# Kernel tuning notes

Measured on AMD Instinct MI355X. Metric: run time of the kernel, lower is better.

The kernel has to match this reference:

```python
import jax, jax.numpy as jnp
import numpy as np

V, E, D, B, T = 50000, 128, 512, 256, 128


def _reverse_seq(x, lengths):
    # TF reverse_sequence: reverse only the valid prefix of each row.
    Tn = x.shape[1]
    t = jnp.arange(Tn)
    idx = jnp.where(t[None, :] < lengths[:, None], lengths[:, None] - 1 - t[None, :], t[None, :])
    return jnp.take_along_axis(x, idx[:, :, None], axis=1)


def _lstm(x, lengths, Wx, Wh, b, reverse):
    # x: [B,T,in]; returns outputs [B,T,D] (zero past length) and final cell state [B,D]
    if reverse:
        x = _reverse_seq(x, lengths)
    Bn, Tn, _ = x.shape
    Dn = Wh.shape[0]
    xg = jnp.einsum('btd,dg->tbg', x, Wx) + b  # [T,B,4D], input projection hoisted out of scan

    def step(carry, inp):
        h, c = carry
        xg_t, t = inp
        gates = xg_t + h @ Wh
        i, j, f, o = jnp.split(gates, 4, axis=-1)  # TF LSTMCell gate order i, j, f, o
        c_new = jax.nn.sigmoid(f + 1.0) * c + jax.nn.sigmoid(i) * jnp.tanh(j)  # forget_bias=1.0
        h_new = jax.nn.sigmoid(o) * jnp.tanh(c_new)
        mask = (t < lengths)[:, None]
        c2 = jnp.where(mask, c_new, c)
        h2 = jnp.where(mask, h_new, h)
        out = jnp.where(mask, h_new, 0.0)  # dynamic_rnn zeros outputs past length
        return (h2, c2), out

    init = (jnp.zeros((Bn, Dn), x.dtype), jnp.zeros((Bn, Dn), x.dtype))
    (h, c), outs = jax.lax.scan(step, init, (xg, jnp.arange(Tn)))
    outs = outs.transpose(1, 0, 2)  # [B,T,D]
    if reverse:
        outs = _reverse_seq(outs, lengths)
    return outs, c


def setup_inputs() -> dict:
    key = jax.random.key(0)
    ks = jax.random.split(key, 20)
    s = 0.05
    inp = {
        'tokens': jax.random.randint(ks[0], (B, T), 0, V, dtype=jnp.int32),
        'lengths': jax.random.randint(ks[1], (B,), 1, T + 1, dtype=jnp.int32),
        'embedding': jax.random.normal(ks[2], (V, E), jnp.float32) * s,
    }
    in_dims = [E, 2 * D]
    k = 3
    for l in range(2):
        for d in ('f', 'b'):
            inp[f'Wx_{d}{l}'] = jax.random.normal(ks[k], (in_dims[l], 4 * D), jnp.float32) * s; k += 1
            inp[f'Wh_{d}{l}'] = jax.random.normal(ks[k], (D, 4 * D), jnp.float32) * s; k += 1
            inp[f'b_{d}{l}'] = jnp.zeros((4 * D,), jnp.float32)
    inp['W_head'] = jax.random.normal(ks[k], (2 * D, D), jnp.float32) * s; k += 1
    inp['b1'] = jnp.zeros((D,), jnp.float32)
    inp['U'] = jax.random.normal(ks[k], (D, V), jnp.float32) * s; k += 1
    inp['b2'] = jnp.zeros((V,), jnp.float32)
    return inp


def reference(tokens, lengths, embedding, Wx_f0, Wh_f0, b_f0, Wx_b0, Wh_b0, b_b0,
              Wx_f1, Wh_f1, b_f1, Wx_b1, Wh_b1, b_b1, W_head, b1, U, b2):
    x = embedding[tokens]  # [B,T,E]
    fw_out, fw_c = _lstm(x, lengths, Wx_f0, Wh_f0, b_f0, reverse=False)
    bw_out, bw_c = _lstm(x, lengths, Wx_b0, Wh_b0, b_b0, reverse=True)
    x = jnp.concatenate([fw_out, bw_out], axis=-1)  # [B,T,2D]
    fw_out, fw_c = _lstm(x, lengths, Wx_f1, Wh_f1, b_f1, reverse=False)
    bw_out, bw_c = _lstm(x, lengths, Wx_b1, Wh_b1, b_b1, reverse=True)
    states = jnp.concatenate([fw_c, bw_c], axis=-1)  # top-layer final cell states [B,2D]
    h = jax.nn.relu(states @ W_head + b1)
    pred = h @ U + b2  # [B,V]
    return pred
```

## Files before the change

kernel.cpp:

```cpp
#include <hip/hip_runtime.h>
#include <hip/hip_bf16.h>
#include <stdint.h>


#define DEV static __device__ __forceinline__

using f32x4 = __attribute__((ext_vector_type(4))) float;
using s16x8 = __attribute__((ext_vector_type(8))) short;
typedef unsigned long long u64;

#define TT 128
#define DD 512
#define VV 50000

#define O_CTR0   ((size_t)0)
#define O_CTR1   ((size_t)2048)
#define O_HG0    ((size_t)4096)
#define SZ_HG    ((size_t)(2*8*64*512*2))
#define O_HG1    (O_HG0 + SZ_HG)
#define O_ZEND   (O_HG1 + SZ_HG)
#define O_XEMB   (O_ZEND)
#define O_W0T    (O_XEMB + (size_t)32768*128*2)
#define O_WH1T   (O_W0T  + (size_t)2*2048*640*2)
#define O_W1XT   (O_WH1T + (size_t)2*2048*512*2)
#define O_WHDT   (O_W1XT + (size_t)4096*1024*2)
#define O_STATES (O_WHDT + (size_t)512*1024*2)
#define O_HHEAD  (O_STATES + (size_t)256*1024*2)
#define O_OUT0   (O_HHEAD + (size_t)256*512*2)
#define O_XG1    (O_OUT0 + (size_t)32768*1024*2)
#define THIN_END (O_XG1 + (size_t)32768*2048*2)
#define FAT_END  (O_XG1 + (size_t)32768*4096*2)

DEV unsigned short f2bf(float f) {
  union { float f; unsigned int u; } a; a.f = f;
  unsigned int r = a.u + 0x7FFFu + ((a.u >> 16) & 1u);
  return (unsigned short)(r >> 16);
}
DEV float bf2f(unsigned short u) {
  union { unsigned int u; float f; } a; a.u = ((unsigned int)u) << 16; return a.f;
}
DEV float sigm(float x)  { return __builtin_amdgcn_rcpf(1.f + __expf(-x)); }
DEV float tanh_(float x) { return 1.f - 2.f * __builtin_amdgcn_rcpf(1.f + __expf(2.f * x)); }

DEV void gload16(const void* g, void* l) {
  __builtin_amdgcn_global_load_lds((const __attribute__((address_space(1))) void*)g,
                                   (__attribute__((address_space(3))) void*)l, 16, 0, 0);
}

__global__ __launch_bounds__(256) void k_embed(const int* __restrict__ tok,
                                               const float* __restrict__ emb,
                                               unsigned short* __restrict__ x) {
  for (int i = blockIdx.x * 256 + threadIdx.x; i < 32768 * 16; i += 256 * 256) {
    int bt = i >> 4, c = i & 15;
    int tk = tok[bt];
    const float* s = emb + (size_t)tk * 128 + c * 8;
    float4 a = *(const float4*)s, b = *(const float4*)(s + 4);
    union { unsigned short us[8]; s16x8 v; } o;
    o.us[0] = f2bf(a.x); o.us[1] = f2bf(a.y); o.us[2] = f2bf(a.z); o.us[3] = f2bf(a.w);
    o.us[4] = f2bf(b.x); o.us[5] = f2bf(b.y); o.us[6] = f2bf(b.z); o.us[7] = f2bf(b.w);
    *(s16x8*)&x[(size_t)bt * 128 + c * 8] = o.v;
  }
}

__global__ __launch_bounds__(256) void k_prep(const float* __restrict__ src,
                                              unsigned short* __restrict__ dst,
                                              int k_off, int src_ld, int K_full,
                                              int perm, int swz) {
  __shared__ __align__(16) unsigned short tile[64][72];
  int n0 = blockIdx.x * 64, k0 = blockIdx.y * 64;
  int t = threadIdx.x;
  for (int r = 0; r < 16; ++r) {
    int kk = r * 4 + (t >> 6);
    int nn = t & 63;
    int n = n0 + nn;
    int col = perm ? (((n >> 4) & 3) * 512 + (n >> 6) * 16 + (n & 15)) : n;
    tile[nn][kk] = f2bf(src[(size_t)(k0 + kk) * src_ld + col]);
  }
  __syncthreads();
  for (int j = 0; j < 2; ++j) {
    int ch = j * 256 + t;
    int nn = ch >> 3, kc = ch & 7;
    s16x8 v = *(const s16x8*)&tile[nn][kc * 8];
    int n = n0 + nn;
    size_t byte = ((size_t)n * K_full + (k_off + k0 + kc * 8)) * 2;
    if (swz) byte ^= (size_t)((n & 7) << 4);
    *(s16x8*)((char*)dst + byte) = v;
  }
}

DEV void poll_ctr(const int* p, int target) {
  if ((threadIdx.x & 63) == 0) {
    int guard = 0;
    while (__hip_atomic_load(p, __ATOMIC_RELAXED, __HIP_MEMORY_SCOPE_AGENT) < target) {
      __builtin_amdgcn_s_sleep(1);
      if (++guard > (1 << 18)) break;
    }
  }
  asm volatile("" ::: "memory");
}
DEV void arrive_ctr(int* p) {
  __syncthreads();
  if (threadIdx.x == 0)
    __hip_atomic_fetch_add(p, 1, __ATOMIC_RELAXED, __HIP_MEMORY_SCOPE_AGENT);
}

DEV u64 hload8(const void* p) {
  return __hip_atomic_load((const u64*)p, __ATOMIC_RELAXED, __HIP_MEMORY_SCOPE_AGENT);
}
DEV void hstore_pair(unsigned short* addr_even, float hv, int lane) {
  unsigned int hb = (unsigned int)f2bf(hv);
  unsigned int pb = __shfl_xor(hb, 1);
  if (!(lane & 1))
    __hip_atomic_store((unsigned int*)addr_even, hb | (pb << 16),
                       __ATOMIC_RELAXED, __HIP_MEMORY_SCOPE_AGENT);
}

__global__ __launch_bounds__(256) void k_lstm0(
    const unsigned short* __restrict__ xemb, const unsigned short* __restrict__ W0T,
    const int* __restrict__ lengths, const float* __restrict__ bf0,
    const float* __restrict__ bb0, unsigned short* __restrict__ hg,
    int* __restrict__ ctr, unsigned short* __restrict__ out0) {
  extern __shared__ char smem[];
  int bid = blockIdx.x;
  int combo = bid & 7, chunk = bid >> 3;
  int dir = combo >> 2, grp = combo & 3;
  int tid = threadIdx.x;
  {
    const char* wsrc = (const char*)W0T + ((size_t)(dir * 2048 + chunk * 64)) * 640 * 2;
    for (int j = 0; j < 20; ++j)
      gload16(wsrc + j * 4096 + tid * 16, smem + j * 4096 + (tid >> 6) * 1024);
  }
  __syncthreads();

  int lane = tid & 63, l15 = lane & 15, lhi = lane >> 4, m = tid >> 6;
  int rowAl = m * 16 + l15;
  int rowA = grp * 64 + rowAl;
  int lenA = lengths[rowA];
  int dim = chunk * 16 + l15;
  const float* bs = dir ? bb0 : bf0;
  float bias[4];
  #pragma unroll
  for (int g = 0; g < 4; ++g) bias[g] = bs[g * 512 + dim];

  int rpl[4], lenP[4];
  #pragma unroll
  for (int r = 0; r < 4; ++r) {
    rpl[r] = m * 16 + lhi * 4 + r;
    lenP[r] = lengths[grp * 64 + rpl[r]];
  }
  float cS[4] = {0.f, 0.f, 0.f, 0.f};
  float hP[4] = {0.f, 0.f, 0.f, 0.f};
  int X = (l15 & 7) << 4;
  int bn[4];
  #pragma unroll
  for (int g = 0; g < 4; ++g) bn[g] = (g * 16 + l15) * 1280 + lhi * 16;
  int* ctr_p = ctr + combo * 16;

  for (int t = 0; t < TT; ++t) {
    int posA = dir ? ((t < lenA) ? lenA - 1 - t : t) : t;
    const char* xb = (const char*)xemb + ((size_t)(rowA * 128 + posA)) * 128 * 2;
    s16x8 xf[4];
    #pragma unroll
    for (int kt = 0; kt < 4; ++kt)
      xf[kt] = *(const s16x8*)(xb + (kt * 32 + lhi * 8) * 2);

    poll_ctr(ctr_p, 32 * t);
    const char* hr = (const char*)hg + ((size_t)((t & 1) * 8 + combo)) * 64 * 512 * 2
                     + (size_t)rowAl * 512 * 2;
    u64 h8[32];
    #pragma unroll
    for (int kt = 0; kt < 16; ++kt) {
      h8[2 * kt]     = hload8(hr + kt * 64 + lhi * 16);
      h8[2 * kt + 1] = hload8(hr + kt * 64 + lhi * 16 + 8);
    }
    f32x4 acc[4] = {};
    #pragma unroll
    for (int kt = 0; kt < 20; ++kt) {
      s16x8 a;
      if (kt < 4) a = xf[kt];
      else { union { u64 q[2]; s16x8 v; } u;
             u.q[0] = h8[2 * (kt - 4)]; u.q[1] = h8[2 * (kt - 4) + 1]; a = u.v; }
      #pragma unroll
      for (int g = 0; g < 4; ++g) {
        s16x8 b = *(const s16x8*)(smem + ((bn[g] + kt * 64) ^ X));
        acc[g] = __builtin_amdgcn_mfma_f32_16x16x32_bf16(a, b, acc[g], 0, 0, 0);
      }
    }
    unsigned short* hw = hg + ((size_t)(((t + 1) & 1) * 8 + combo)) * 64 * 512;
    #pragma unroll
    for (int r = 0; r < 4; ++r) {
      float gi = acc[0][r] + bias[0];
      float gj = acc[1][r] + bias[1];
      float gf = acc[2][r] + bias[2];
      float go = acc[3][r] + bias[3];
      float cn = sigm(gf + 1.f) * cS[r] + sigm(gi) * tanh_(gj);
      float hn = sigm(go) * tanh_(cn);
      int act = (t < lenP[r]);
      cS[r] = act ? cn : cS[r];
      float hv = act ? hn : hP[r];
      hP[r] = hv;
      hstore_pair(&hw[rpl[r] * 512 + (dim & ~1)], hv, lane);
      int b = grp * 64 + rpl[r];
      int posP = dir ? ((act) ? lenP[r] - 1 - t : t) : t;
      out0[((size_t)b * 128 + posP) * 1024 + dir * 512 + dim] = f2bf(act ? hn : 0.f);
    }
    arrive_ctr(ctr_p);
  }
}

__global__ __launch_bounds__(256) void k_lstm1(
    const unsigned short* __restrict__ xg, int ldxg, int dircolmul,
    const unsigned short* __restrict__ Wh1T, const int* __restrict__ lengths,
    const float* __restrict__ bf1, const float* __restrict__ bb1,
    unsigned short* __restrict__ hg, int* __restrict__ ctr,
    unsigned short* __restrict__ states, int dirFixed) {
  extern __shared__ char smem[];
  int bid = blockIdx.x;
  int dir, grp, chunk;
  if (dirFixed >= 0) { dir = dirFixed; grp = bid & 3; chunk = bid >> 2; }
  else               { dir = (bid & 7) >> 2; grp = bid & 3; chunk = bid >> 3; }
  int combo = dir * 4 + grp;
  int tid = threadIdx.x;
  {
    const char* wsrc = (const char*)Wh1T + ((size_t)(dir * 2048 + chunk * 64)) * 512 * 2;
    for (int j = 0; j < 16; ++j)
      gload16(wsrc + j * 4096 + tid * 16, smem + j * 4096 + (tid >> 6) * 1024);
  }
  __syncthreads();

  int lane = tid & 63, l15 = lane & 15, lhi = lane >> 4, m = tid >> 6;
  int rowAl = m * 16 + l15;
  int dim = chunk * 16 + l15;
  const float* bs = dir ? bb1 : bf1;
  float bias[4];
  #pragma unroll
  for (int g = 0; g < 4; ++g) bias[g] = bs[g * 512 + dim];
  int rpl[4], lenP[4], bG[4];
  #pragma unroll
  for (int r = 0; r < 4; ++r) {
    rpl[r] = m * 16 + lhi * 4 + r;
    bG[r] = grp * 64 + rpl[r];
    lenP[r] = lengths[bG[r]];
  }
  float cS[4] = {0.f, 0.f, 0.f, 0.f};
  float hP[4] = {0.f, 0.f, 0.f, 0.f};
  int X = (l15 & 7) << 4;
  int bn[4];
  #pragma unroll
  for (int g = 0; g < 4; ++g) bn[g] = (g * 16 + l15) * 1024 + lhi * 16;
  int* ctr_p = ctr + combo * 16;
  int colbase = dircolmul * dir + chunk * 64 + l15;

  for (int t = 0; t < TT; ++t) {
    unsigned short xv[4][4];
    #pragma unroll
    for (int r = 0; r < 4; ++r) {
      int posP = dir ? ((t < lenP[r]) ? lenP[r] - 1 - t : t) : t;
      size_t rowoff = ((size_t)bG[r] * 128 + posP) * ldxg + colbase;
      #pragma unroll
      for (int g = 0; g < 4; ++g) xv[g][r] = xg[rowoff + g * 16];
    }
    poll_ctr(ctr_p, 32 * t);
    const char* hr = (const char*)hg + ((size_t)((t & 1) * 8 + combo)) * 64 * 512 * 2
                     + (size_t)rowAl * 512 * 2;
    u64 h8[32];
    #pragma unroll
    for (int kt = 0; kt < 16; ++kt) {
      h8[2 * kt]     = hload8(hr + kt * 64 + lhi * 16);
      h8[2 * kt + 1] = hload8(hr + kt * 64 + lhi * 16 + 8);
    }
    f32x4 acc[4] = {};
    #pragma unroll
    for (int kt = 0; kt < 16; ++kt) {
      union { u64 q[2]; s16x8 v; } u;
      u.q[0] = h8[2 * kt]; u.q[1] = h8[2 * kt + 1];
      s16x8 a = u.v;
      #pragma unroll
      for (int g = 0; g < 4; ++g) {
        s16x8 b = *(const s16x8*)(smem + ((bn[g] + kt * 64) ^ X));
        acc[g] = __builtin_amdgcn_mfma_f32_16x16x32_bf16(a, b, acc[g], 0, 0, 0);
      }
    }
    unsigned short* hw = hg + ((size_t)(((t + 1) & 1) * 8 + combo)) * 64 * 512;
    #pragma unroll
    for (int r = 0; r < 4; ++r) {
      float gi = acc[0][r] + bias[0] + bf2f(xv[0][r]);
      float gj = acc[1][r] + bias[1] + bf2f(xv[1][r]);
      float gf = acc[2][r] + bias[2] + bf2f(xv[2][r]);
      float go = acc[3][r] + bias[3] + bf2f(xv[3][r]);
      float cn = sigm(gf + 1.f) * cS[r] + sigm(gi) * tanh_(gj);
      float hn = sigm(go) * tanh_(cn);
      int act = (t < lenP[r]);
      cS[r] = act ? cn : cS[r];
      float hv = act ? hn : hP[r];
      hP[r] = hv;
      hstore_pair(&hw[rpl[r] * 512 + (dim & ~1)], hv, lane);
    }
    arrive_ctr(ctr_p);
  }
  #pragma unroll
  for (int r = 0; r < 4; ++r)
    states[(size_t)bG[r] * 1024 + dir * 512 + dim] = f2bf(cS[r]);
}

__global__ __launch_bounds__(256) void k_gemm(const unsigned short* __restrict__ A,
                                              const unsigned short* __restrict__ Bt,
                                              unsigned short* __restrict__ C,
                                              int K, int ldc, int mode,
                                              const float* __restrict__ bias) {
  __shared__ __align__(16) char gs[65536];
  int m0 = blockIdx.x * 128, n0 = blockIdx.y * 128;
  int tid = threadIdx.x, lane = tid & 63, l15 = lane & 15, lhi = lane >> 4;
  int w = tid >> 6, wrow = w >> 1, wcol = w & 1;
  f32x4 acc[4][4] = {};
  int nk = K >> 6;

  auto stage = [&](int buf, int ki) {
    const char* As = (const char*)A + ((size_t)m0 * K + ki * 64) * 2;
    const char* Bs = (const char*)Bt + ((size_t)n0 * K + ki * 64) * 2;
    for (int j = 0; j < 4; ++j) {
      int fb = j * 4096 + tid * 16;
      int row = fb >> 7, inrow = fb & 127;
      gload16(As + (size_t)row * K * 2 + inrow, gs + buf * 16384 + j * 4096 + (tid >> 6) * 1024);
      gload16(Bs + (size_t)row * K * 2 + inrow, gs + 32768 + buf * 16384 + j * 4096 + (tid >> 6) * 1024);
    }
  };
  stage(0, 0);
  __syncthreads();
  for (int ki = 0; ki < nk; ++ki) {
    int buf = ki & 1;
    if (ki + 1 < nk) stage(buf ^ 1, ki + 1);
    const char* sa = gs + buf * 16384;
    const char* sb = gs + 32768 + buf * 16384;
    #pragma unroll
    for (int kt = 0; kt < 2; ++kt) {
      s16x8 af[4];
      #pragma unroll
      for (int mt = 0; mt < 4; ++mt)
        af[mt] = *(const s16x8*)(sa + ((wrow * 64 + mt * 16 + l15) * 128 + kt * 64 + lhi * 16));
      #pragma unroll
      for (int nt = 0; nt < 4; ++nt) {
        s16x8 bf_ = *(const s16x8*)(sb + ((wcol * 64 + nt * 16 + l15) * 128 + kt * 64 + lhi * 16));
        #pragma unroll
        for (int mt = 0; mt < 4; ++mt)
          acc[mt][nt] = __builtin_amdgcn_mfma_f32_16x16x32_bf16(af[mt], bf_, acc[mt][nt], 0, 0, 0);
      }
    }
    __syncthreads();
  }
  #pragma unroll
  for (int mt = 0; mt < 4; ++mt)
    #pragma unroll
    for (int nt = 0; nt < 4; ++nt)
      #pragma unroll
      for (int r = 0; r < 4; ++r) {
        int row = m0 + wrow * 64 + mt * 16 + lhi * 4 + r;
        int col = n0 + wcol * 64 + nt * 16 + l15;
        float v = acc[mt][nt][r];
        if (mode) { v += bias[col]; v = fmaxf(v, 0.f); }
        C[(size_t)row * ldc + col] = f2bf(v);
      }
}

__global__ __launch_bounds__(256) void k_pred(const unsigned short* __restrict__ hh,
                                              const float* __restrict__ U,
                                              const float* __restrict__ b2,
                                              float* __restrict__ out) {
  __shared__ __align__(16) char ps[65536];
  int n0 = blockIdx.x * 128;
  int tid = threadIdx.x, lane = tid & 63, l15 = lane & 15, lhi = lane >> 4, w = tid >> 6;
  f32x4 acc[4][8] = {};
  unsigned short* tb = (unsigned short*)(ps + 32768);
  bool full = (n0 + 128) <= VV;

  for (int ki = 0; ki < 8; ++ki) {
    int k0 = ki * 64;
    const char* As = (const char*)hh + (size_t)k0 * 2;
    for (int j = 0; j < 8; ++j) {
      int fb = j * 4096 + tid * 16;
      int row = fb >> 7, inrow = fb & 127;
      gload16(As + (size_t)row * 512 * 2 + inrow, ps + j * 4096 + (tid >> 6) * 1024);
    }
    for (int c8 = 0; c8 < 8; ++c8) {
      int flat = c8 * 1024 + tid * 4;
      int kk = flat >> 7, nn = flat & 127;
      float v0, v1, v2, v3;
      if (full) {
        float4 v = *(const float4*)(U + (size_t)(k0 + kk) * VV + (n0 + nn));
        v0 = v.x; v1 = v.y; v2 = v.z; v3 = v.w;
      } else {
        v0 = (n0 + nn + 0 < VV) ? U[(size_t)(k0 + kk) * VV + n0 + nn + 0] : 0.f;
        v1 = (n0 + nn + 1 < VV) ? U[(size_t)(k0 + kk) * VV + n0 + nn + 1] : 0.f;
        v2 = (n0 + nn + 2 < VV) ? U[(size_t)(k0 + kk) * VV + n0 + nn + 2] : 0.f;
        v3 = (n0 + nn + 3 < VV) ? U[(size_t)(k0 + kk) * VV + n0 + nn + 3] : 0.f;
      }
      tb[(nn + 0) * 72 + kk] = f2bf(v0);
      tb[(nn + 1) * 72 + kk] = f2bf(v1);
      tb[(nn + 2) * 72 + kk] = f2bf(v2);
      tb[(nn + 3) * 72 + kk] = f2bf(v3);
    }
    __syncthreads();
    #pragma unroll
    for (int kt = 0; kt < 2; ++kt) {
      s16x8 af[4];
      #pragma unroll
      for (int mt = 0; mt < 4; ++mt)
        af[mt] = *(const s16x8*)(ps + ((w * 64 + mt * 16 + l15) * 128 + kt * 64 + lhi * 16));
      #pragma unroll
      for (int nt = 0; nt < 8; ++nt) {
        s16x8 bf_ = *(const s16x8*)((char*)tb + ((nt * 16 + l15) * 144 + kt * 64 + lhi * 16));
        #pragma unroll
        for (int mt = 0; mt < 4; ++mt)
          acc[mt][nt] = __builtin_amdgcn_mfma_f32_16x16x32_bf16(af[mt], bf_, acc[mt][nt], 0, 0, 0);
      }
    }
    __syncthreads();
  }
  #pragma unroll
  for (int nt = 0; nt < 8; ++nt) {
    int col = n0 + nt * 16 + l15;
    float bv = (col < VV) ? b2[col] : 0.f;
    #pragma unroll
    for (int mt = 0; mt < 4; ++mt)
      #pragma unroll
      for (int r = 0; r < 4; ++r) {
        int row = w * 64 + mt * 16 + lhi * 4 + r;
        if (col < VV) out[(size_t)row * VV + col] = acc[mt][nt][r] + bv;
      }
  }
}

extern "C" void kernel_launch(void* const* d_in, const int* in_sizes, int n_in,
                              void* d_out, int out_size, void* d_ws, size_t ws_size,
                              hipStream_t stream) {
  const int* tokens = (const int*)d_in[0];
  const int* lengths = (const int*)d_in[1];
  const float* emb   = (const float*)d_in[2];
  const float* Wx_f0 = (const float*)d_in[3];
  const float* Wh_f0 = (const float*)d_in[4];
  const float* b_f0  = (const float*)d_in[5];
  const float* Wx_b0 = (const float*)d_in[6];
  const float* Wh_b0 = (const float*)d_in[7];
  const float* b_b0  = (const float*)d_in[8];
  const float* Wx_f1 = (const float*)d_in[9];
  const float* Wh_f1 = (const float*)d_in[10];
  const float* b_f1  = (const float*)d_in[11];
  const float* Wx_b1 = (const float*)d_in[12];
  const float* Wh_b1 = (const float*)d_in[13];
  const float* b_b1  = (const float*)d_in[14];
  const float* W_head = (const float*)d_in[15];
  const float* b1    = (const float*)d_in[16];
  const float* U     = (const float*)d_in[17];
  const float* b2    = (const float*)d_in[18];

  if (ws_size < (size_t)THIN_END) return;

  char* ws = (char*)d_ws;
  int* ctr0 = (int*)(ws + O_CTR0);
  int* ctr1 = (int*)(ws + O_CTR1);
  unsigned short* hg0   = (unsigned short*)(ws + O_HG0);
  unsigned short* hg1   = (unsigned short*)(ws + O_HG1);
  unsigned short* xemb  = (unsigned short*)(ws + O_XEMB);
  unsigned short* W0T   = (unsigned short*)(ws + O_W0T);
  unsigned short* WH1T  = (unsigned short*)(ws + O_WH1T);
  unsigned short* W1XT  = (unsigned short*)(ws + O_W1XT);
  unsigned short* WHDT  = (unsigned short*)(ws + O_WHDT);
  unsigned short* states = (unsigned short*)(ws + O_STATES);
  unsigned short* hhead = (unsigned short*)(ws + O_HHEAD);
  unsigned short* out0  = (unsigned short*)(ws + O_OUT0);
  unsigned short* xg1   = (unsigned short*)(ws + O_XG1);

  bool fat = (ws_size >= (size_t)FAT_END);

  hipFuncSetAttribute((const void*)k_lstm0, hipFuncAttributeMaxDynamicSharedMemorySize, 81920);
  hipFuncSetAttribute((const void*)k_lstm1, hipFuncAttributeMaxDynamicSharedMemorySize, 65536);

  hipMemsetAsync(ws, 0, O_ZEND, stream);

  k_embed<<<dim3(256), dim3(256), 0, stream>>>(tokens, emb, xemb);

  k_prep<<<dim3(32, 2), 256, 0, stream>>>(Wx_f0, W0T,               0,   2048, 640, 1, 1);
  k_prep<<<dim3(32, 8), 256, 0, stream>>>(Wh_f0, W0T,               128, 2048, 640, 1, 1);
  k_prep<<<dim3(32, 2), 256, 0, stream>>>(Wx_b0, W0T + 2048 * 640,  0,   2048, 640, 1, 1);
  k_prep<<<dim3(32, 8), 256, 0, stream>>>(Wh_b0, W0T + 2048 * 640,  128, 2048, 640, 1, 1);
  k_prep<<<dim3(32, 8), 256, 0, stream>>>(Wh_f1, WH1T,              0,   2048, 512, 1, 1);
  k_prep<<<dim3(32, 8), 256, 0, stream>>>(Wh_b1, WH1T + 2048 * 512, 0,   2048, 512, 1, 1);
  k_prep<<<dim3(32, 16), 256, 0, stream>>>(Wx_f1, W1XT,               0, 2048, 1024, 1, 0);
  k_prep<<<dim3(32, 16), 256, 0, stream>>>(Wx_b1, W1XT + 2048 * 1024, 0, 2048, 1024, 1, 0);
  k_prep<<<dim3(8, 16), 256, 0, stream>>>(W_head, WHDT,              0,  512, 1024, 0, 0);

  k_lstm0<<<256, 256, 81920, stream>>>(xemb, W0T, lengths, b_f0, b_b0, hg0, ctr0, out0);

  if (fat) {
    k_gemm<<<dim3(256, 32), 256, 0, stream>>>(out0, W1XT, xg1, 1024, 4096, 0, nullptr);
    k_lstm1<<<256, 256, 65536, stream>>>(xg1, 4096, 2048, WH1T, lengths, b_f1, b_b1,
                                         hg1, ctr1, states, -1);
  } else {
    k_gemm<<<dim3(256, 16), 256, 0, stream>>>(out0, W1XT, xg1, 1024, 2048, 0, nullptr);
    k_lstm1<<<128, 256, 65536, stream>>>(xg1, 2048, 0, WH1T, lengths, b_f1, b_b1,
                                         hg1, ctr1, states, 0);
    k_gemm<<<dim3(256, 16), 256, 0, stream>>>(out0, W1XT + (size_t)2048 * 1024, xg1,
                                              1024, 2048, 0, nullptr);
    k_lstm1<<<128, 256, 65536, stream>>>(xg1, 2048, 0, WH1T, lengths, b_f1, b_b1,
                                         hg1, ctr1, states, 1);
  }

  k_gemm<<<dim3(2, 4), 256, 0, stream>>>(states, WHDT, hhead, 1024, 512, 1, b1);
  k_pred<<<dim3(391), 256, 0, stream>>>(hhead, U, b2, (float*)d_out);
}
```

Baseline: 2.260 ms.

## Replace counter barrier with per-wave flag sync and pack layer-1 gate loads

The shared atomic counter with block-wide syncthreads is replaced by per-wave, per-chunk flags that are stored after a vmcnt wait and polled with a wave-wide all-reduce. Each wave now waits only on the matching wave rows from other chunks, not on a whole-block barrier. The out0 store in layer 0 is moved after the flag publish, taking it off the critical path. The layer-1 input-projection weights are permuted so each lane's four gate values sit next to each other and can be fetched with one 64-bit load instead of 16 scalar loads. The risks are heavier polling traffic from 32 lanes spinning without sleep, and the correctness of the relaxed-ordering memory visibility.

```diff
diff --git a/kernel.cpp b/kernel.cpp
--- a/kernel.cpp
+++ b/kernel.cpp
@@ -14,8 +14,8 @@
 #define VV 50000
 
 #define O_CTR0   ((size_t)0)
-#define O_CTR1   ((size_t)2048)
-#define O_HG0    ((size_t)4096)
+#define O_CTR1   ((size_t)4096)
+#define O_HG0    ((size_t)8192)
 #define SZ_HG    ((size_t)(2*8*64*512*2))
 #define O_HG1    (O_HG0 + SZ_HG)
 #define O_ZEND   (O_HG1 + SZ_HG)
@@ -73,7 +73,9 @@
     int kk = r * 4 + (t >> 6);
     int nn = t & 63;
     int n = n0 + nn;
-    int col = perm ? (((n >> 4) & 3) * 512 + (n >> 6) * 16 + (n & 15)) : n;
+    int col = n;
+    if (perm == 1) col = ((n >> 4) & 3) * 512 + (n >> 6) * 16 + (n & 15);
+    if (perm == 2) col = (n & 3) * 512 + (n >> 6) * 16 + ((n >> 2) & 15);
     tile[nn][kk] = f2bf(src[(size_t)(k0 + kk) * src_ld + col]);
   }
   __syncthreads();
@@ -88,20 +90,20 @@
   }
 }
 
-DEV void poll_ctr(const int* p, int target) {
-  if ((threadIdx.x & 63) == 0) {
-    int guard = 0;
-    while (__hip_atomic_load(p, __ATOMIC_RELAXED, __HIP_MEMORY_SCOPE_AGENT) < target) {
-      __builtin_amdgcn_s_sleep(1);
-      if (++guard > (1 << 18)) break;
-    }
+DEV void poll_flags(const int* fbase, int target) {
+  const int* p = fbase + (threadIdx.x & 31);
+  int guard = 0;
+  for (;;) {
+    int v = __hip_atomic_load(p, __ATOMIC_RELAXED, __HIP_MEMORY_SCOPE_AGENT);
+    if (__all(v >= target)) break;
+    if (++guard > (1 << 18)) break;
   }
   asm volatile("" ::: "memory");
 }
-DEV void arrive_ctr(int* p) {
-  __syncthreads();
-  if (threadIdx.x == 0)
-    __hip_atomic_fetch_add(p, 1, __ATOMIC_RELAXED, __HIP_MEMORY_SCOPE_AGENT);
+DEV void set_flag(int* fp, int v, int lane) {
+  asm volatile("s_waitcnt vmcnt(0)" ::: "memory");
+  if (lane == 0)
+    __hip_atomic_store(fp, v, __ATOMIC_RELAXED, __HIP_MEMORY_SCOPE_AGENT);
 }
 
 DEV u64 hload8(const void* p) {
@@ -119,7 +121,7 @@
     const unsigned short* __restrict__ xemb, const unsigned short* __restrict__ W0T,
     const int* __restrict__ lengths, const float* __restrict__ bf0,
     const float* __restrict__ bb0, unsigned short* __restrict__ hg,
-    int* __restrict__ ctr, unsigned short* __restrict__ out0) {
+    int* __restrict__ flags, unsigned short* __restrict__ out0) {
   extern __shared__ char smem[];
   int bid = blockIdx.x;
   int combo = bid & 7, chunk = bid >> 3;
@@ -154,7 +156,8 @@
   int bn[4];
   #pragma unroll
   for (int g = 0; g < 4; ++g) bn[g] = (g * 16 + l15) * 1280 + lhi * 16;
-  int* ctr_p = ctr + combo * 16;
+  int* fbase = flags + (combo * 4 + m) * 32;
+  int* fown  = fbase + chunk;
 
   for (int t = 0; t < TT; ++t) {
     int posA = dir ? ((t < lenA) ? lenA - 1 - t : t) : t;
@@ -164,7 +167,7 @@
     for (int kt = 0; kt < 4; ++kt)
       xf[kt] = *(const s16x8*)(xb + (kt * 32 + lhi * 8) * 2);
 
-    poll_ctr(ctr_p, 32 * t);
+    poll_flags(fbase, t);
     const char* hr = (const char*)hg + ((size_t)((t & 1) * 8 + combo)) * 64 * 512 * 2
                      + (size_t)rowAl * 512 * 2;
     u64 h8[32];
@@ -187,6 +190,7 @@
       }
     }
     unsigned short* hw = hg + ((size_t)(((t + 1) & 1) * 8 + combo)) * 64 * 512;
+    float hnv[4]; int actv[4];
     #pragma unroll
     for (int r = 0; r < 4; ++r) {
       float gi = acc[0][r] + bias[0];
@@ -196,15 +200,19 @@
       float cn = sigm(gf + 1.f) * cS[r] + sigm(gi) * tanh_(gj);
       float hn = sigm(go) * tanh_(cn);
       int act = (t < lenP[r]);
+      hnv[r] = hn; actv[r] = act;
       cS[r] = act ? cn : cS[r];
       float hv = act ? hn : hP[r];
       hP[r] = hv;
       hstore_pair(&hw[rpl[r] * 512 + (dim & ~1)], hv, lane);
+    }
+    set_flag(fown, t + 1, lane);
+    #pragma unroll
+    for (int r = 0; r < 4; ++r) {
       int b = grp * 64 + rpl[r];
-      int posP = dir ? ((act) ? lenP[r] - 1 - t : t) : t;
-      out0[((size_t)b * 128 + posP) * 1024 + dir * 512 + dim] = f2bf(act ? hn : 0.f);
-    }
-    arrive_ctr(ctr_p);
+      int posP = dir ? (actv[r] ? lenP[r] - 1 - t : t) : t;
+      out0[((size_t)b * 128 + posP) * 1024 + dir * 512 + dim] = f2bf(actv[r] ? hnv[r] : 0.f);
+    }
   }
 }
 
@@ -212,7 +220,7 @@
     const unsigned short* __restrict__ xg, int ldxg, int dircolmul,
     const unsigned short* __restrict__ Wh1T, const int* __restrict__ lengths,
     const float* __restrict__ bf1, const float* __restrict__ bb1,
-    unsigned short* __restrict__ hg, int* __restrict__ ctr,
+    unsigned short* __restrict__ hg, int* __restrict__ flags,
     unsigned short* __restrict__ states, int dirFixed) {
   extern __shared__ char smem[];
   int bid = blockIdx.x;
@@ -248,19 +256,18 @@
   int bn[4];
   #pragma unroll
   for (int g = 0; g < 4; ++g) bn[g] = (g * 16 + l15) * 1024 + lhi * 16;
-  int* ctr_p = ctr + combo * 16;
-  int colbase = dircolmul * dir + chunk * 64 + l15;
+  int* fbase = flags + (combo * 4 + m) * 32;
+  int* fown  = fbase + chunk;
+  int colbase = dircolmul * dir + chunk * 64 + l15 * 4;
 
   for (int t = 0; t < TT; ++t) {
-    unsigned short xv[4][4];
+    u64 xq[4];
     #pragma unroll
     for (int r = 0; r < 4; ++r) {
       int posP = dir ? ((t < lenP[r]) ? lenP[r] - 1 - t : t) : t;
-      size_t rowoff = ((size_t)bG[r] * 128 + posP) * ldxg + colbase;
-      #pragma unroll
-      for (int g = 0; g < 4; ++g) xv[g][r] = xg[rowoff + g * 16];
-    }
-    poll_ctr(ctr_p, 32 * t);
+      xq[r] = *(const u64*)&xg[((size_t)bG[r] * 128 + posP) * ldxg + colbase];
+    }
+    poll_flags(fbase, t);
     const char* hr = (const char*)hg + ((size_t)((t & 1) * 8 + combo)) * 64 * 512 * 2
                      + (size_t)rowAl * 512 * 2;
     u64 h8[32];
@@ -284,10 +291,10 @@
     unsigned short* hw = hg + ((size_t)(((t + 1) & 1) * 8 + combo)) * 64 * 512;
     #pragma unroll
     for (int r = 0; r < 4; ++r) {
-      float gi = acc[0][r] + bias[0] + bf2f(xv[0][r]);
-      float gj = acc[1][r] + bias[1] + bf2f(xv[1][r]);
-      float gf = acc[2][r] + bias[2] + bf2f(xv[2][r]);
-      float go = acc[3][r] + bias[3] + bf2f(xv[3][r]);
+      float gi = acc[0][r] + bias[0] + bf2f((unsigned short)(xq[r]       & 0xFFFF));
+      float gj = acc[1][r] + bias[1] + bf2f((unsigned short)((xq[r]>>16) & 0xFFFF));
+      float gf = acc[2][r] + bias[2] + bf2f((unsigned short)((xq[r]>>32) & 0xFFFF));
+      float go = acc[3][r] + bias[3] + bf2f((unsigned short)((xq[r]>>48) & 0xFFFF));
       float cn = sigm(gf + 1.f) * cS[r] + sigm(gi) * tanh_(gj);
       float hn = sigm(go) * tanh_(cn);
       int act = (t < lenP[r]);
@@ -296,7 +303,7 @@
       hP[r] = hv;
       hstore_pair(&hw[rpl[r] * 512 + (dim & ~1)], hv, lane);
     }
-    arrive_ctr(ctr_p);
+    set_flag(fown, t + 1, lane);
   }
   #pragma unroll
   for (int r = 0; r < 4; ++r)
@@ -485,8 +492,8 @@
   k_prep<<<dim3(32, 8), 256, 0, stream>>>(Wh_b0, W0T + 2048 * 640,  128, 2048, 640, 1, 1);
   k_prep<<<dim3(32, 8), 256, 0, stream>>>(Wh_f1, WH1T,              0,   2048, 512, 1, 1);
   k_prep<<<dim3(32, 8), 256, 0, stream>>>(Wh_b1, WH1T + 2048 * 512, 0,   2048, 512, 1, 1);
-  k_prep<<<dim3(32, 16), 256, 0, stream>>>(Wx_f1, W1XT,               0, 2048, 1024, 1, 0);
-  k_prep<<<dim3(32, 16), 256, 0, stream>>>(Wx_b1, W1XT + 2048 * 1024, 0, 2048, 1024, 1, 0);
+  k_prep<<<dim3(32, 16), 256, 0, stream>>>(Wx_f1, W1XT,               0, 2048, 1024, 2, 0);
+  k_prep<<<dim3(32, 16), 256, 0, stream>>>(Wx_b1, W1XT + 2048 * 1024, 0, 2048, 1024, 2, 0);
   k_prep<<<dim3(8, 16), 256, 0, stream>>>(W_head, WHDT,              0,  512, 1024, 0, 0);
 
   k_lstm0<<<256, 256, 81920, stream>>>(xemb, W0T, lengths, b_f0, b_b0, hg0, ctr0, out0);
```

Result: slower. 2.709 ms (+19.9%).
